# Kernel tuning notes

Hardware: AMD Instinct MI355X
Metric: run time of the kernel (lower is better)

The kernel has to match this reference:

```python
import math
import jax, jax.numpy as jnp
import numpy as np

H = 16          # head_count
DM = 1024       # model_dim
D = DM // H     # dim_per_head = 64
B, SL, CL = 2, 1024, 512


def setup_inputs() -> dict:
    key = jax.random.key(0)
    ks = jax.random.split(key, 16)
    s = 0.02  # weight init scale
    def W(k):
        return jax.random.normal(k, (DM, DM), jnp.float32) * s
    def b(k):
        return jax.random.normal(k, (DM,), jnp.float32) * s
    return {
        "self_kvq": jax.random.normal(ks[0], (B, SL, DM), jnp.float32),
        "ctx_kv": jax.random.normal(ks[1], (B, CL, DM), jnp.float32),
        "self_mask": jax.random.bernoulli(ks[2], 0.1, (B, SL, SL)),
        "ctx_mask": jax.random.bernoulli(ks[3], 0.1, (B, 1, CL)),
        "Wq": W(ks[4]), "bq": b(ks[5]),
        "Wks": W(ks[6]), "bks": b(ks[7]),
        "Wvs": W(ks[8]), "bvs": b(ks[9]),
        "Wkc": W(ks[10]), "bkc": b(ks[11]),
        "Wvc": W(ks[12]), "bvc": b(ks[13]),
        "ctx_bias": jnp.full((1,), -10.0, jnp.float32),  # Parameter(ones(1) * -10)
        "Wo": W(ks[14]), "bo": b(ks[15]),
    }


def reference(self_kvq, ctx_kv, self_mask, ctx_mask,
              Wq, bq, Wks, bks, Wvs, bvs, Wkc, bkc, Wvc, bvc,
              ctx_bias, Wo, bo):
    Bx, self_len, _ = self_kvq.shape
    ctx_len = ctx_kv.shape[1]

    def shape4(x):  # (B, L, DM) -> (B, H, L, D)
        return x.reshape(Bx, -1, H, D).transpose(0, 2, 1, 3)

    query = shape4(self_kvq @ Wq.T + bq) / math.sqrt(D)
    key = shape4(jnp.concatenate([self_kvq @ Wks.T + bks, ctx_kv @ Wkc.T + bkc], axis=1))
    value = shape4(jnp.concatenate([self_kvq @ Wvs.T + bvs, ctx_kv @ Wvc.T + bvc], axis=1))

    scores = jnp.einsum('bhqd,bhkd->bhqk', query, key)
    # ctx_weight_param: add learned bias to the context segment of the scores
    kidx = jnp.arange(self_len + ctx_len)
    scores = scores + jnp.where(kidx >= self_len, ctx_bias[0], jnp.zeros((), scores.dtype))
    scores = scores.astype(jnp.float32)

    # self_mask: (B, Q, self_len) -> (B, 1, Q, self_len); ctx_mask: (B, 1, ctx_len) -> (B, 1, Q, ctx_len)
    full_mask = jnp.concatenate([
        jnp.broadcast_to(self_mask[:, None], (Bx, 1, self_len, self_len)),
        jnp.broadcast_to(ctx_mask[:, None], (Bx, 1, self_len, ctx_len)),
    ], axis=-1)
    scores = jnp.where(full_mask, jnp.float32(-1e18), scores)

    attn = jax.nn.softmax(scores, axis=-1).astype(query.dtype)
    # dropout p=0.0 -> identity
    context = jnp.einsum('bhqk,bhkd->bhqd', attn, value)
    context = context.transpose(0, 2, 1, 3).reshape(Bx, self_len, H * D)
    output = context @ Wo.T + bo

    ctx_attn_probs = attn[..., self_len:]
    ctx_attn_probs = ctx_attn_probs / ctx_attn_probs.sum(axis=-1, keepdims=True)
    top_attn = ctx_attn_probs[:, 0]  # head 0: (B, Q, ctx_len)
    return output, top_attn, attn
```

## Files before the change

### kernel.cpp

```cpp
#include <hip/hip_runtime.h>
#include <cstdint>

constexpr int H  = 16;
constexpr int D  = 64;
constexpr int DM = 1024;
constexpr int B  = 2;
constexpr int SL = 1024;
constexpr int CL = 512;
constexpr int KL = SL + CL;
constexpr int EPAD = 1540;
constexpr size_t M1 = 1u << 20;

typedef short bf16x8  __attribute__((ext_vector_type(8)));
typedef float f32x4   __attribute__((ext_vector_type(4)));
typedef short short4v __attribute__((ext_vector_type(4)));

__device__ __forceinline__ short f2b(float f) {
    uint32_t u = __float_as_uint(f);
    u = (u + 0x7fffu + ((u >> 16) & 1u)) >> 16;
    return (short)u;
}

__device__ __forceinline__ bf16x8 ld8(const unsigned short* p) {
    return *reinterpret_cast<const bf16x8*>(p);
}

__device__ __forceinline__ void async16(const void* g, void* l) {
    __builtin_amdgcn_global_load_lds(
        (const __attribute__((address_space(1))) void*)g,
        (__attribute__((address_space(3))) void*)l,
        16, 0, 0);
}

struct ConvSrc { const float* p[8]; };

__global__ __launch_bounds__(256)
void convert_kernel(ConvSrc srcs, unsigned short* __restrict__ dst)
{
    size_t i8 = (size_t)blockIdx.x * 256 + threadIdx.x;
    size_t e  = i8 * 8;
    int u = (int)(e >> 20);
    const float* s; size_t off;
    if (u < 2) { s = srcs.p[0]; off = e; }
    else       { s = srcs.p[u - 1]; off = e - ((size_t)u << 20); }
    float4 a = *reinterpret_cast<const float4*>(s + off);
    float4 b = *reinterpret_cast<const float4*>(s + off + 4);
    bf16x8 r;
    r[0]=f2b(a.x); r[1]=f2b(a.y); r[2]=f2b(a.z); r[3]=f2b(a.w);
    r[4]=f2b(b.x); r[5]=f2b(b.y); r[6]=f2b(b.z); r[7]=f2b(b.w);
    *reinterpret_cast<bf16x8*>(dst + e) = r;
}

template<int MODE, int RPB_SHIFT, int OUTLEN, int ROWOFF>
__device__ __forceinline__ void gemm_body(
    const unsigned short* __restrict__ A,
    const unsigned short* __restrict__ W,
    const float* __restrict__ bias,
    void* __restrict__ outp, float scale,
    unsigned short* sA, unsigned short* sB, int by, int bx)
{
    const int t   = threadIdx.x;
    const int l   = t & 63;
    const int wid = t >> 6;
    const int lr  = l & 15, lg = l >> 4;
    const int mbase = by * 64;
    const int nbase = bx * 128;

    f32x4 acc[4][2] = {};
    for (int k0 = 0; k0 < DM; k0 += 64) {
        #pragma unroll
        for (int i = 0; i < 2; ++i) {
            int c = t + 256 * i;
            int row = c >> 3, gd = (c & 7) ^ (row & 7);
            async16(A + (size_t)(mbase + row) * DM + k0 + gd * 8, sA + c * 8);
        }
        #pragma unroll
        for (int i = 0; i < 4; ++i) {
            int c = t + 256 * i;
            int row = c >> 3, gd = (c & 7) ^ (row & 7);
            async16(W + (size_t)(nbase + row) * DM + k0 + gd * 8, sB + c * 8);
        }
        __syncthreads();
        bf16x8 af[4][2], bfr[2][2];
        #pragma unroll
        for (int s = 0; s < 2; ++s) {
            #pragma unroll
            for (int i = 0; i < 4; ++i) {
                int row = i * 16 + lr;
                af[i][s] = ld8(sA + (row * 8 + ((s * 4 + lg) ^ (row & 7))) * 8);
            }
            #pragma unroll
            for (int j = 0; j < 2; ++j) {
                int row = wid * 32 + j * 16 + lr;
                bfr[j][s] = ld8(sB + (row * 8 + ((s * 4 + lg) ^ (row & 7))) * 8);
            }
        }
        #pragma unroll
        for (int s = 0; s < 2; ++s)
            #pragma unroll
            for (int i = 0; i < 4; ++i)
                #pragma unroll
                for (int j = 0; j < 2; ++j)
                    acc[i][j] = __builtin_amdgcn_mfma_f32_16x16x32_bf16(af[i][s], bfr[j][s], acc[i][j], 0, 0, 0);
        __syncthreads();
    }

    #pragma unroll
    for (int mi = 0; mi < 4; ++mi) {
        #pragma unroll
        for (int nj = 0; nj < 2; ++nj) {
            int n = nbase + wid * 32 + nj * 16 + lr;
            float bi = bias[n];
            if (MODE == 1) {
                int m0 = mbase + mi * 16 + lg * 4;
                int bb = m0 >> RPB_SHIFT;
                int s0 = m0 & ((1 << RPB_SHIFT) - 1);
                int hh = n >> 6, dd = n & 63;
                unsigned short* o = (unsigned short*)outp +
                    ((size_t)(bb * H + hh) * D + dd) * KL + ROWOFF + s0;
                short4v pk;
                #pragma unroll
                for (int r = 0; r < 4; ++r) pk[r] = f2b((acc[mi][nj][r] + bi) * scale);
                *reinterpret_cast<short4v*>(o) = pk;
            } else {
                #pragma unroll
                for (int r = 0; r < 4; ++r) {
                    int m = mbase + mi * 16 + lg * 4 + r;
                    float v = (acc[mi][nj][r] + bi) * scale;
                    if (MODE == 0) {
                        int bb = m >> RPB_SHIFT;
                        int s  = m & ((1 << RPB_SHIFT) - 1);
                        int hh = n >> 6, dd = n & 63;
                        ((unsigned short*)outp)[((size_t)(bb * H + hh) * OUTLEN + ROWOFF + s) * D + dd]
                            = (unsigned short)f2b(v);
                    } else {
                        __builtin_nontemporal_store(v, (float*)outp + (size_t)m * DM + n);
                    }
                }
            }
        }
    }
}

__global__ __launch_bounds__(256)
void proj_kernel(const unsigned short* __restrict__ Aself,
                 const unsigned short* __restrict__ Actx,
                 const unsigned short* __restrict__ Wq,
                 const unsigned short* __restrict__ Wks,
                 const unsigned short* __restrict__ Wvs,
                 const unsigned short* __restrict__ Wkc,
                 const unsigned short* __restrict__ Wvc,
                 const float* __restrict__ bq,  const float* __restrict__ bks,
                 const float* __restrict__ bvs, const float* __restrict__ bkc,
                 const float* __restrict__ bvc,
                 unsigned short* __restrict__ q_ws,
                 unsigned short* __restrict__ k_ws,
                 unsigned short* __restrict__ vT_ws)
{
    __shared__ unsigned short sA[64 * 64];
    __shared__ unsigned short sB[128 * 64];
    int bid = blockIdx.x;
    int z, by, bx;
    if (bid < 768) { z = bid >> 8; int r = bid & 255; by = r >> 3; bx = r & 7; }
    else { int tt = bid - 768; z = 3 + (tt >> 7); int r = tt & 127; by = r >> 3; bx = r & 7; }
    if (z == 0)
        gemm_body<0, 10, SL, 0 >(Aself, Wq,  bq,  q_ws,  0.125f, sA, sB, by, bx);
    else if (z == 1)
        gemm_body<0, 10, KL, 0 >(Aself, Wks, bks, k_ws,  1.0f,   sA, sB, by, bx);
    else if (z == 2)
        gemm_body<1, 10, 0,  0 >(Aself, Wvs, bvs, vT_ws, 1.0f,   sA, sB, by, bx);
    else if (z == 3)
        gemm_body<0, 9,  KL, SL>(Actx,  Wkc, bkc, k_ws,  1.0f,   sA, sB, by, bx);
    else
        gemm_body<1, 9,  0,  SL>(Actx,  Wvc, bvc, vT_ws, 1.0f,   sA, sB, by, bx);
}

__global__ __launch_bounds__(256)
void out_proj_kernel(const unsigned short* __restrict__ ctx_bf,
                     const unsigned short* __restrict__ Wo,
                     const float* __restrict__ bo,
                     float* __restrict__ out0)
{
    __shared__ unsigned short sA[64 * 64];
    __shared__ unsigned short sB[128 * 64];
    gemm_body<2, 10, 0, 0>(ctx_bf, Wo, bo, out0, 1.0f, sA, sB, blockIdx.y, blockIdx.x);
}

__global__ __launch_bounds__(512, 4)
void attn_kernel(const unsigned short* __restrict__ q_ws,
                 const unsigned short* __restrict__ k_ws,
                 const unsigned short* __restrict__ vT_ws,
                 const int* __restrict__ self_mask,
                 const int* __restrict__ ctx_mask,
                 const float* __restrict__ ctx_bias,
                 float* __restrict__ attn_out,
                 float* __restrict__ top_out,
                 unsigned short* __restrict__ ctx_ws)
{
    __shared__ unsigned short e_lds[16 * EPAD];
    __shared__ float s_part[16 * 64];
    __shared__ unsigned int mb[16 * 48];
    __shared__ float wred[16 * 8 * 3];
    __shared__ float fin[16 * 3];

    const int bid = blockIdx.x;
    const int bh  = bid & 31;
    const int qt  = bid >> 5;
    const int b   = bh >> 4;
    const int h   = bh & 15;
    const int t   = threadIdx.x;
    const int l   = t & 63;
    const int wid = t >> 6;
    const int lr  = l & 15;
    const int lg  = l >> 4;
    const int qrow0 = qt * 16;

    {
        int row = t >> 5, w = t & 31;
        const int4* p = (const int4*)(self_mask + ((size_t)b * SL + qrow0 + row) * SL + w * 32);
        unsigned bits = 0;
        #pragma unroll
        for (int g = 0; g < 8; ++g) {
            int4 v = p[g];
            bits |= (unsigned)(v.x != 0) << (g * 4);
            bits |= (unsigned)(v.y != 0) << (g * 4 + 1);
            bits |= (unsigned)(v.z != 0) << (g * 4 + 2);
            bits |= (unsigned)(v.w != 0) << (g * 4 + 3);
        }
        mb[row * 48 + w] = bits;
    }
    if (t < 256) {
        int row = t >> 4, w = t & 15;
        const int4* p = (const int4*)(ctx_mask + (size_t)b * CL + w * 32);
        unsigned bits = 0;
        #pragma unroll
        for (int g = 0; g < 8; ++g) {
            int4 v = p[g];
            bits |= (unsigned)(v.x != 0) << (g * 4);
            bits |= (unsigned)(v.y != 0) << (g * 4 + 1);
            bits |= (unsigned)(v.z != 0) << (g * 4 + 2);
            bits |= (unsigned)(v.w != 0) << (g * 4 + 3);
        }
        mb[row * 48 + 32 + w] = bits;
    }
    s_part[t] = 0.f;
    s_part[t + 512] = 0.f;

    const unsigned short* qb = q_ws + ((size_t)bh * SL + qrow0) * D;
    const unsigned short* kb = k_ws + (size_t)bh * KL * D;
    const float cb = ctx_bias[0];
    bf16x8 aq0 = ld8(qb + lr * D + lg * 8);
    bf16x8 aq1 = ld8(qb + lr * D + 32 + lg * 8);
    __syncthreads();

    float m[4], sa[4], sc[4];
    #pragma unroll
    for (int r = 0; r < 4; ++r) { m[r] = -3.0e38f; sa[r] = 0.f; sc[r] = 0.f; }

    for (int jj = 0; jj < 12; ++jj) {
        int j = wid * 12 + jj;
        int col = j * 16 + lr;
        bf16x8 bk0 = ld8(kb + (size_t)col * D + lg * 8);
        bf16x8 bk1 = ld8(kb + (size_t)col * D + 32 + lg * 8);
        f32x4 c = {};
        c = __builtin_amdgcn_mfma_f32_16x16x32_bf16(aq0, bk0, c, 0, 0, 0);
        c = __builtin_amdgcn_mfma_f32_16x16x32_bf16(aq1, bk1, c, 0, 0, 0);
        const int isctx = (col >= SL);
        const int wi = col >> 5, bit = col & 31;
        #pragma unroll
        for (int r = 0; r < 4; ++r) {
            int row = lg * 4 + r;
            float v = c[r] + (isctx ? cb : 0.f);
            if ((mb[row * 48 + wi] >> bit) & 1u) v = -1e30f;
            float nm = fmaxf(m[r], v);
            float rs = __expf(m[r] - nm);
            float ev = __expf(v - nm);
            sa[r] = sa[r] * rs + ev;
            sc[r] = sc[r] * rs + (isctx ? ev : 0.f);
            m[r]  = nm;
        }
    }
    #pragma unroll
    for (int off = 1; off < 16; off <<= 1) {
        #pragma unroll
        for (int r = 0; r < 4; ++r) {
            float om = __shfl_xor(m[r], off);
            float os = __shfl_xor(sa[r], off);
            float oc = __shfl_xor(sc[r], off);
            float nm = fmaxf(m[r], om);
            float e1 = __expf(m[r] - nm), e2 = __expf(om - nm);
            sa[r] = sa[r] * e1 + os * e2;
            sc[r] = sc[r] * e1 + oc * e2;
            m[r]  = nm;
        }
    }
    if (lr == 0) {
        #pragma unroll
        for (int r = 0; r < 4; ++r) {
            int row = lg * 4 + r;
            wred[(row * 8 + wid) * 3 + 0] = m[r];
            wred[(row * 8 + wid) * 3 + 1] = sa[r];
            wred[(row * 8 + wid) * 3 + 2] = sc[r];
        }
    }
    __syncthreads();
    if (t < 16) {
        float fm = -3.0e38f, fs = 0.f, fc = 0.f;
        #pragma unroll
        for (int w = 0; w < 8; ++w) {
            float wm = wred[(t * 8 + w) * 3 + 0];
            float ws = wred[(t * 8 + w) * 3 + 1];
            float wc = wred[(t * 8 + w) * 3 + 2];
            float nm = fmaxf(fm, wm);
            float e1 = __expf(fm - nm), e2 = __expf(wm - nm);
            fs = fs * e1 + ws * e2;
            fc = fc * e1 + wc * e2;
            fm = nm;
        }
        fin[t * 3 + 0] = fm;
        fin[t * 3 + 1] = 1.0f / fs;
        fin[t * 3 + 2] = 1.0f / fc;
    }
    __syncthreads();

    float* aout = attn_out + ((size_t)bh * SL + qrow0) * KL;
    float* tout = top_out + ((size_t)b * SL + qrow0) * CL;
    for (int jj = 0; jj < 12; ++jj) {
        int j = wid * 12 + jj;
        int col = j * 16 + lr;
        bf16x8 bk0 = ld8(kb + (size_t)col * D + lg * 8);
        bf16x8 bk1 = ld8(kb + (size_t)col * D + 32 + lg * 8);
        f32x4 c = {};
        c = __builtin_amdgcn_mfma_f32_16x16x32_bf16(aq0, bk0, c, 0, 0, 0);
        c = __builtin_amdgcn_mfma_f32_16x16x32_bf16(aq1, bk1, c, 0, 0, 0);
        const int isctx = (col >= SL);
        const int wi = col >> 5, bit = col & 31;
        #pragma unroll
        for (int r = 0; r < 4; ++r) {
            int row = lg * 4 + r;
            float v = c[r] + (isctx ? cb : 0.f);
            if ((mb[row * 48 + wi] >> bit) & 1u) v = -1e30f;
            float ev = __expf(v - fin[row * 3 + 0]);
            float p  = ev * fin[row * 3 + 1];
            __builtin_nontemporal_store(p, aout + (size_t)row * KL + col);
            e_lds[row * EPAD + col] = (unsigned short)f2b(p);
            if (h == 0 && isctx) {
                float tp = ev * fin[row * 3 + 2];
                __builtin_nontemporal_store(tp, tout + (size_t)row * CL + (col - SL));
            }
        }
    }
    __syncthreads();

    const unsigned short* vb = vT_ws + (size_t)bh * D * KL;
    f32x4 accv[4] = {};
    for (int ks = 0; ks < 6; ++ks) {
        int k0 = wid * 192 + ks * 32;
        bf16x8 ap = ld8(e_lds + lr * EPAD + k0 + lg * 8);
        #pragma unroll
        for (int df = 0; df < 4; ++df) {
            bf16x8 bv = ld8(vb + (size_t)(df * 16 + lr) * KL + k0 + lg * 8);
            accv[df] = __builtin_amdgcn_mfma_f32_16x16x32_bf16(ap, bv, accv[df], 0, 0, 0);
        }
    }
    #pragma unroll
    for (int df = 0; df < 4; ++df)
        #pragma unroll
        for (int r = 0; r < 4; ++r)
            atomicAdd(&s_part[(lg * 4 + r) * 64 + df * 16 + lr], accv[df][r]);
    __syncthreads();

    for (int i = t; i < 1024; i += 512) {
        int srow = i >> 6, dd = i & 63;
        ctx_ws[((size_t)b * SL + qrow0 + srow) * DM + h * D + dd]
            = (unsigned short)f2b(s_part[i]);
    }
}

extern "C" void kernel_launch(void* const* d_in, const int* in_sizes, int n_in,
                              void* d_out, int out_size, void* d_ws, size_t ws_size,
                              hipStream_t stream)
{
    const float* self_kvq = (const float*)d_in[0];
    const float* ctx_kv   = (const float*)d_in[1];
    const int*   self_mask= (const int*)d_in[2];
    const int*   ctx_mask = (const int*)d_in[3];
    const float* Wq  = (const float*)d_in[4];
    const float* bq  = (const float*)d_in[5];
    const float* Wks = (const float*)d_in[6];
    const float* bks = (const float*)d_in[7];
    const float* Wvs = (const float*)d_in[8];
    const float* bvs = (const float*)d_in[9];
    const float* Wkc = (const float*)d_in[10];
    const float* bkc = (const float*)d_in[11];
    const float* Wvc = (const float*)d_in[12];
    const float* bvc = (const float*)d_in[13];
    const float* ctx_bias = (const float*)d_in[14];
    const float* Wo  = (const float*)d_in[15];
    const float* bo  = (const float*)d_in[16];

    float* out0     = (float*)d_out;
    float* out_top  = out0 + (size_t)B * SL * DM;
    float* out_attn = out_top + (size_t)B * SL * CL;

    unsigned short* wsp  = (unsigned short*)d_ws;
    unsigned short* Abf_self = wsp + 0 * M1;
    unsigned short* Abf_ctx  = wsp + 2 * M1;
    unsigned short* Wq_b     = wsp + 3 * M1;
    unsigned short* Wks_b    = wsp + 4 * M1;
    unsigned short* Wvs_b    = wsp + 5 * M1;
    unsigned short* Wkc_b    = wsp + 6 * M1;
    unsigned short* Wvc_b    = wsp + 7 * M1;
    unsigned short* Wo_b     = wsp + 8 * M1;
    unsigned short* q_ws     = wsp + 9 * M1;
    unsigned short* k_ws     = wsp + 11 * M1;
    unsigned short* vT_ws    = wsp + 14 * M1;
    unsigned short* ctx_ws   = wsp + 0;

    ConvSrc cs;
    cs.p[0] = self_kvq; cs.p[1] = ctx_kv;
    cs.p[2] = Wq; cs.p[3] = Wks; cs.p[4] = Wvs;
    cs.p[5] = Wkc; cs.p[6] = Wvc; cs.p[7] = Wo;
    convert_kernel<<<4608, 256, 0, stream>>>(cs, wsp);

    proj_kernel<<<dim3(1024), 256, 0, stream>>>(
        Abf_self, Abf_ctx, Wq_b, Wks_b, Wvs_b, Wkc_b, Wvc_b,
        bq, bks, bvs, bkc, bvc, q_ws, k_ws, vT_ws);

    attn_kernel<<<dim3(2048), 512, 0, stream>>>(q_ws, k_ws, vT_ws,
        self_mask, ctx_mask, ctx_bias, out_attn, out_top, ctx_ws);

    out_proj_kernel<<<dim3(8, 32), 256, 0, stream>>>(ctx_ws, Wo_b, bo, out0);
}
```

Before: 526.9 us.

## Keep attention scores in registers instead of recomputing QK^T in second pass

```diff
diff --git a/kernel.cpp b/kernel.cpp
--- a/kernel.cpp
+++ b/kernel.cpp
@@ -8,7 +8,7 @@
 constexpr int SL = 1024;
 constexpr int CL = 512;
 constexpr int KL = SL + CL;
-constexpr int EPAD = 1540;
+constexpr int EPAD = 1544;
 constexpr size_t M1 = 1u << 20;
 
 typedef short bf16x8  __attribute__((ext_vector_type(8)));
@@ -200,8 +200,9 @@
     __shared__ unsigned short e_lds[16 * EPAD];
     __shared__ float s_part[16 * 64];
     __shared__ unsigned int mb[16 * 48];
-    __shared__ float wred[16 * 8 * 3];
-    __shared__ float fin[16 * 3];
+    __shared__ float wredm[16 * 8];
+    __shared__ float wreds[16 * 8];
+    __shared__ float wredc[16 * 8];
 
     const int bid = blockIdx.x;
     const int bh  = bid & 31;
@@ -253,100 +254,114 @@
     bf16x8 aq1 = ld8(qb + lr * D + 32 + lg * 8);
     __syncthreads();
 
-    float m[4], sa[4], sc[4];
-    #pragma unroll
-    for (int r = 0; r < 4; ++r) { m[r] = -3.0e38f; sa[r] = 0.f; sc[r] = 0.f; }
-
+    f32x4 c[12];
+    float m[4] = {-3.0e38f, -3.0e38f, -3.0e38f, -3.0e38f};
+    #pragma unroll
     for (int jj = 0; jj < 12; ++jj) {
         int j = wid * 12 + jj;
         int col = j * 16 + lr;
         bf16x8 bk0 = ld8(kb + (size_t)col * D + lg * 8);
         bf16x8 bk1 = ld8(kb + (size_t)col * D + 32 + lg * 8);
-        f32x4 c = {};
-        c = __builtin_amdgcn_mfma_f32_16x16x32_bf16(aq0, bk0, c, 0, 0, 0);
-        c = __builtin_amdgcn_mfma_f32_16x16x32_bf16(aq1, bk1, c, 0, 0, 0);
-        const int isctx = (col >= SL);
-        const int wi = col >> 5, bit = col & 31;
+        f32x4 cc = {};
+        cc = __builtin_amdgcn_mfma_f32_16x16x32_bf16(aq0, bk0, cc, 0, 0, 0);
+        cc = __builtin_amdgcn_mfma_f32_16x16x32_bf16(aq1, bk1, cc, 0, 0, 0);
+        const int isctx = (j >= 64);
+        const int wi = j >> 1, bit = (j & 1) * 16 + lr;
         #pragma unroll
         for (int r = 0; r < 4; ++r) {
             int row = lg * 4 + r;
-            float v = c[r] + (isctx ? cb : 0.f);
+            float v = cc[r] + (isctx ? cb : 0.f);
             if ((mb[row * 48 + wi] >> bit) & 1u) v = -1e30f;
-            float nm = fmaxf(m[r], v);
-            float rs = __expf(m[r] - nm);
-            float ev = __expf(v - nm);
-            sa[r] = sa[r] * rs + ev;
-            sc[r] = sc[r] * rs + (isctx ? ev : 0.f);
-            m[r]  = nm;
-        }
-    }
-    #pragma unroll
-    for (int off = 1; off < 16; off <<= 1) {
+            cc[r] = v;
+            m[r] = fmaxf(m[r], v);
+        }
+        c[jj] = cc;
+    }
+
+    #pragma unroll
+    for (int off = 1; off < 16; off <<= 1)
+        #pragma unroll
+        for (int r = 0; r < 4; ++r)
+            m[r] = fmaxf(m[r], __shfl_xor(m[r], off));
+    if (lr == 0) {
+        #pragma unroll
+        for (int r = 0; r < 4; ++r)
+            wredm[(lg * 4 + r) * 8 + wid] = m[r];
+    }
+    __syncthreads();
+
+    float gm[4];
+    #pragma unroll
+    for (int r = 0; r < 4; ++r) {
+        int row = lg * 4 + r;
+        float v = wredm[row * 8 + 0];
+        #pragma unroll
+        for (int w = 1; w < 8; ++w) v = fmaxf(v, wredm[row * 8 + w]);
+        gm[r] = v;
+    }
+
+    float sum[4] = {0.f, 0.f, 0.f, 0.f}, csum[4] = {0.f, 0.f, 0.f, 0.f};
+    #pragma unroll
+    for (int jj = 0; jj < 12; ++jj) {
+        const int isctx = (wid * 12 + jj >= 64);
         #pragma unroll
         for (int r = 0; r < 4; ++r) {
-            float om = __shfl_xor(m[r], off);
-            float os = __shfl_xor(sa[r], off);
-            float oc = __shfl_xor(sc[r], off);
-            float nm = fmaxf(m[r], om);
-            float e1 = __expf(m[r] - nm), e2 = __expf(om - nm);
-            sa[r] = sa[r] * e1 + os * e2;
-            sc[r] = sc[r] * e1 + oc * e2;
-            m[r]  = nm;
-        }
-    }
+            float e = __expf(c[jj][r] - gm[r]);
+            c[jj][r] = e;
+            sum[r] += e;
+            if (isctx) csum[r] += e;
+        }
+    }
+    #pragma unroll
+    for (int off = 1; off < 16; off <<= 1)
+        #pragma unroll
+        for (int r = 0; r < 4; ++r) {
+            sum[r]  += __shfl_xor(sum[r], off);
+            csum[r] += __shfl_xor(csum[r], off);
+        }
     if (lr == 0) {
+        #pragma unroll
+        for (int r = 0; r < 4; ++r) {
+            wreds[(lg * 4 + r) * 8 + wid] = sum[r];
+            wredc[(lg * 4 + r) * 8 + wid] = csum[r];
+        }
+    }
+    __syncthreads();
+
+    float rden[4], rcs[4];
+    #pragma unroll
+    for (int r = 0; r < 4; ++r) {
+        int row = lg * 4 + r;
+        float s = 0.f, cs = 0.f;
+        #pragma unroll
+        for (int w = 0; w < 8; ++w) { s += wreds[row * 8 + w]; cs += wredc[row * 8 + w]; }
+        rden[r] = 1.0f / s;
+        rcs[r]  = 1.0f / cs;
+    }
+
+    float* aout = attn_out + ((size_t)bh * SL + qrow0) * KL;
+    float* tout = top_out + ((size_t)b * SL + qrow0) * CL;
+    #pragma unroll
+    for (int r = 0; r < 4; ++r) {
+        int row = lg * 4 + r;
+        float* arow = aout + (size_t)row * KL;
+        #pragma unroll
+        for (int jj = 0; jj < 12; ++jj) {
+            int col = (wid * 12 + jj) * 16 + lr;
+            float p = c[jj][r] * rden[r];
+            arow[col] = p;
+            e_lds[row * EPAD + col] = (unsigned short)f2b(p);
+        }
+    }
+    if (h == 0) {
         #pragma unroll
         for (int r = 0; r < 4; ++r) {
             int row = lg * 4 + r;
-            wred[(row * 8 + wid) * 3 + 0] = m[r];
-            wred[(row * 8 + wid) * 3 + 1] = sa[r];
-            wred[(row * 8 + wid) * 3 + 2] = sc[r];
-        }
-    }
-    __syncthreads();
-    if (t < 16) {
-        float fm = -3.0e38f, fs = 0.f, fc = 0.f;
-        #pragma unroll
-        for (int w = 0; w < 8; ++w) {
-            float wm = wred[(t * 8 + w) * 3 + 0];
-            float ws = wred[(t * 8 + w) * 3 + 1];
-            float wc = wred[(t * 8 + w) * 3 + 2];
-            float nm = fmaxf(fm, wm);
-            float e1 = __expf(fm - nm), e2 = __expf(wm - nm);
-            fs = fs * e1 + ws * e2;
-            fc = fc * e1 + wc * e2;
-            fm = nm;
-        }
-        fin[t * 3 + 0] = fm;
-        fin[t * 3 + 1] = 1.0f / fs;
-        fin[t * 3 + 2] = 1.0f / fc;
-    }
-    __syncthreads();
-
-    float* aout = attn_out + ((size_t)bh * SL + qrow0) * KL;
-    float* tout = top_out + ((size_t)b * SL + qrow0) * CL;
-    for (int jj = 0; jj < 12; ++jj) {
-        int j = wid * 12 + jj;
-        int col = j * 16 + lr;
-        bf16x8 bk0 = ld8(kb + (size_t)col * D + lg * 8);
-        bf16x8 bk1 = ld8(kb + (size_t)col * D + 32 + lg * 8);
-        f32x4 c = {};
-        c = __builtin_amdgcn_mfma_f32_16x16x32_bf16(aq0, bk0, c, 0, 0, 0);
-        c = __builtin_amdgcn_mfma_f32_16x16x32_bf16(aq1, bk1, c, 0, 0, 0);
-        const int isctx = (col >= SL);
-        const int wi = col >> 5, bit = col & 31;
-        #pragma unroll
-        for (int r = 0; r < 4; ++r) {
-            int row = lg * 4 + r;
-            float v = c[r] + (isctx ? cb : 0.f);
-            if ((mb[row * 48 + wi] >> bit) & 1u) v = -1e30f;
-            float ev = __expf(v - fin[row * 3 + 0]);
-            float p  = ev * fin[row * 3 + 1];
-            __builtin_nontemporal_store(p, aout + (size_t)row * KL + col);
-            e_lds[row * EPAD + col] = (unsigned short)f2b(p);
-            if (h == 0 && isctx) {
-                float tp = ev * fin[row * 3 + 2];
-                __builtin_nontemporal_store(tp, tout + (size_t)row * CL + (col - SL));
+            float* trow = tout + (size_t)row * CL;
+            #pragma unroll
+            for (int jj = 0; jj < 12; ++jj) {
+                int j = wid * 12 + jj;
+                if (j >= 64) trow[j * 16 + lr - SL] = c[jj][r] * rcs[r];
             }
         }
     }
```

Measured after the change: 488.3 us. 1.08x faster.
